# Kernel tuning notes

Hardware: AMD Instinct MI355X
Metric: run time of the kernel (lower is better)

Reference implementation:

```python
import math
import jax, jax.numpy as jnp
import numpy as np

HALF_PI = math.pi / 2
TWOR_SCALE = 1.0 / math.log(2.0)
B, C, L, K = 32, 2, 262144, 4


def setup_inputs() -> dict:
    key = jax.random.key(0)
    ks = jax.random.split(key, 6)
    return {
        "input_signal": jax.random.normal(ks[0], (B, C, L), jnp.float32),
        "twoR": jax.random.normal(ks[1], (B, K), jnp.float32),
        "G": jax.random.normal(ks[2], (B, K), jnp.float32),
        "c_hp": jax.random.normal(ks[3], (B, K), jnp.float32),
        "c_bp": jax.random.normal(ks[4], (B, K), jnp.float32),
        "c_lp": jax.random.normal(ks[5], (B, K), jnp.float32),
    }


def get_biquad_coefficients(twoR, G, c_hp, c_bp, c_lp):
    # each arg: (B, K)
    G2 = G * G
    b0 = c_hp + c_bp * G + c_lp * G2
    b1 = -2.0 * c_hp + 2.0 * c_lp * G2
    b2 = c_hp - c_bp * G + c_lp * G2
    a0 = 1.0 + G2 + twoR * G
    a1 = 2.0 * G2 - 2.0
    a2 = 1.0 + G2 - twoR * G
    return jnp.stack([b0, b1, b2], -1), jnp.stack([a0, a1, a2], -1)  # (B,K,3)


def _biquad_cascade(x, Bs, As):
    # x: (B,C,L); Bs, As: (B,1,K,3) -- broadcast over channels.
    # Direct-form II transposed, cascaded in series over K filters.
    Bs = Bs / As[..., :1]
    As = As / As[..., :1]
    b_, c_ = x.shape[0], x.shape[1]
    y = x
    num_filters = Bs.shape[2]
    for k in range(num_filters):
        b0, b1, b2 = Bs[:, :, k, 0], Bs[:, :, k, 1], Bs[:, :, k, 2]  # (B,1)
        a1, a2 = As[:, :, k, 1], As[:, :, k, 2]  # (B,1)

        def step(carry, xt):
            s1, s2 = carry
            yt = b0 * xt + s1              # (B,C)
            s1n = b1 * xt - a1 * yt + s2
            s2n = b2 * xt - a2 * yt
            return (s1n, s2n), yt

        init = (jnp.zeros((b_, c_), y.dtype), jnp.zeros((b_, c_), y.dtype))
        _, yT = jax.lax.scan(step, init, jnp.moveaxis(y, -1, 0))  # (L,B,C)
        y = jnp.moveaxis(yT, 0, -1)
    return y


def reference(input_signal, twoR, G, c_hp, c_bp, c_lp):
    G = jnp.tan(HALF_PI * jax.nn.sigmoid(G))
    twoR = TWOR_SCALE * jax.nn.softplus(twoR) + 0.01
    Bs, As = get_biquad_coefficients(twoR, G, c_hp, c_bp, c_lp)  # (B,K,3)
    Bs, As = Bs[:, None], As[:, None]  # unsqueeze(1): (B,1,K,3)
    return _biquad_cascade(input_signal, Bs, As)
```

## Files before the change

kernel.cpp:

```cpp
#include <hip/hip_runtime.h>
#include <math.h>

#define B_N 32
#define C_N 2
#define L_N 262144
#define K_N 4
#define NSEQ (B_N * C_N)
#define CHUNK 64
#define THREADS 128
#define BLKSAMP (CHUNK * THREADS)
#define NBLK_SEQ (L_N / BLKSAMP)
#define NBLK_TOT (NSEQ * NBLK_SEQ)
#define NLVL 7
#define ROWP (CHUNK + 1)

#define WS_COEF 0
#define WS_PL   (B_N * 20)
#define WS_PBLK (WS_PL + B_N * NLVL * 64)
#define WS_AGG  (WS_PBLK + B_N * 64)

__global__ __launch_bounds__(64) void svf_prep(
    const float* __restrict__ twoR, const float* __restrict__ Graw,
    const float* __restrict__ c_hp, const float* __restrict__ c_bp,
    const float* __restrict__ c_lp, float* __restrict__ ws)
{
    const int b = blockIdx.x;
    const int t = threadIdx.x;
    __shared__ double cf[K_N][5];
    __shared__ double M[8][8];

    if (t < K_N) {
        const int k = t;
        double g  = (double)Graw[b * K_N + k];
        double tr = (double)twoR[b * K_N + k];
        double hp = (double)c_hp[b * K_N + k];
        double bp = (double)c_bp[b * K_N + k];
        double lp = (double)c_lp[b * K_N + k];
        double sg = 1.0 / (1.0 + exp(-g));
        double G  = tan(1.5707963267948966 * sg);
        double R  = log1p(exp(tr)) * 1.4426950408889634 + 0.01;
        double G2 = G * G;
        double b0 = hp + bp * G + lp * G2;
        double b1 = -2.0 * hp + 2.0 * lp * G2;
        double b2 = hp - bp * G + lp * G2;
        double a0 = 1.0 + G2 + R * G;
        double a1 = 2.0 * G2 - 2.0;
        double a2 = 1.0 + G2 - R * G;
        cf[k][0] = b0 / a0; cf[k][1] = b1 / a0; cf[k][2] = b2 / a0;
        cf[k][3] = a1 / a0; cf[k][4] = a2 / a0;
    }
    __syncthreads();

    if (t < 20) ws[WS_COEF + b * 20 + t] = (float)cf[t / 5][t % 5];

    if (t < 8) {
        double s[8];
        #pragma unroll
        for (int i = 0; i < 8; ++i) s[i] = (i == t) ? 1.0 : 0.0;
        double in = 0.0;
        #pragma unroll
        for (int k = 0; k < K_N; ++k) {
            double y   = cf[k][0] * in + s[2 * k];
            double s1n = cf[k][1] * in - cf[k][3] * y + s[2 * k + 1];
            double s2n = cf[k][2] * in - cf[k][4] * y;
            s[2 * k] = s1n; s[2 * k + 1] = s2n; in = y;
        }
        #pragma unroll
        for (int i = 0; i < 8; ++i) M[i][t] = s[i];
    }
    __syncthreads();

    const int i = t >> 3, j = t & 7;
    for (int p = 1; p <= 13; ++p) {
        double acc = 0.0;
        #pragma unroll
        for (int k = 0; k < 8; ++k) acc += M[i][k] * M[k][j];
        __syncthreads();
        M[i][j] = acc;
        __syncthreads();
        if (p >= 6 && p <= 12) ws[WS_PL + (b * NLVL + (p - 6)) * 64 + t] = (float)acc;
        if (p == 13)           ws[WS_PBLK + b * 64 + t] = (float)acc;
    }
}

__device__ __forceinline__ float cascade_step(const float cf[20], float s[8], float in)
{
    #pragma unroll
    for (int k = 0; k < K_N; ++k) {
        float y  = fmaf(cf[k * 5 + 0], in, s[2 * k]);
        float t1 = fmaf(cf[k * 5 + 1], in, s[2 * k + 1]);
        float n1 = fmaf(-cf[k * 5 + 3], y, t1);
        float n2 = fmaf(-cf[k * 5 + 4], y, cf[k * 5 + 2] * in);
        s[2 * k] = n1; s[2 * k + 1] = n2;
        in = y;
    }
    return in;
}

__device__ __forceinline__ void load_tile(const float* __restrict__ xg,
                                          float* __restrict__ xt, int tid)
{
    #pragma unroll
    for (int k = 0; k < BLKSAMP / 4 / THREADS; ++k) {
        const int g0 = (tid + k * THREADS) * 4;
        float4 v = ((const float4*)xg)[tid + k * THREADS];
        const int a = (g0 >> 6) * ROWP + (g0 & 63);
        xt[a] = v.x; xt[a + 1] = v.y; xt[a + 2] = v.z; xt[a + 3] = v.w;
    }
}

__global__ __launch_bounds__(THREADS) void svf_pass1(
    const float* __restrict__ x, const float* __restrict__ ws,
    float* __restrict__ out)
{
    const int seq = blockIdx.x >> 5;
    const int blk = blockIdx.x & (NBLK_SEQ - 1);
    const int tid = threadIdx.x;
    const int b   = seq >> 1;

    __shared__ float xt[THREADS * ROWP];
    __shared__ float Pm[NLVL][64];
    __shared__ float tb[THREADS][9];

    for (int q = tid; q < NLVL * 64; q += THREADS)
        Pm[q >> 6][q & 63] = ws[WS_PL + b * NLVL * 64 + q];

    float cf[20];
    #pragma unroll
    for (int q = 0; q < 20; ++q) cf[q] = ws[WS_COEF + b * 20 + q];

    const size_t base = (size_t)seq * L_N + (size_t)blk * BLKSAMP;
    load_tile(x + base, xt, tid);
    __syncthreads();

    float t[8] = {0, 0, 0, 0, 0, 0, 0, 0};
    const float* xr = &xt[tid * ROWP];
    #pragma unroll 4
    for (int j = 0; j < CHUNK; ++j) (void)cascade_step(cf, t, xr[j]);

    for (int l = 0; l < NLVL; ++l) {
        const int d = 1 << l;
        #pragma unroll
        for (int q = 0; q < 8; ++q) tb[tid][q] = t[q];
        __syncthreads();
        float prev[8];
        const bool have = (tid >= d);
        if (have) {
            #pragma unroll
            for (int q = 0; q < 8; ++q) prev[q] = tb[tid - d][q];
        }
        __syncthreads();
        if (have) {
            #pragma unroll
            for (int r = 0; r < 8; ++r) {
                float acc = t[r];
                #pragma unroll
                for (int c = 0; c < 8; ++c)
                    acc = fmaf(Pm[l][r * 8 + c], prev[c], acc);
                t[r] = acc;
            }
        }
    }

    float e[8] = {0, 0, 0, 0, 0, 0, 0, 0};
    if (tid > 0) {
        #pragma unroll
        for (int q = 0; q < 8; ++q) e[q] = tb[tid - 1][q];
    }
    float4* eo = (float4*)(out + base);
    eo[2 * tid]     = make_float4(e[0], e[1], e[2], e[3]);
    eo[2 * tid + 1] = make_float4(e[4], e[5], e[6], e[7]);

    if (tid == THREADS - 1) {
        float* agg = (float*)ws + WS_AGG + (size_t)blockIdx.x * 8;
        #pragma unroll
        for (int q = 0; q < 8; ++q) agg[q] = t[q];
    }
}

__global__ __launch_bounds__(64) void svf_scanb(float* __restrict__ ws)
{
    const int seq = threadIdx.x;
    const int b   = seq >> 1;
    float P[64];
    #pragma unroll
    for (int q = 0; q < 64; ++q) P[q] = ws[WS_PBLK + b * 64 + q];

    float* agg = ws + WS_AGG + (size_t)seq * NBLK_SEQ * 8;

    float t[8] = {0, 0, 0, 0, 0, 0, 0, 0};
    for (int j = 0; j < NBLK_SEQ; ++j) {
        float f[8];
        #pragma unroll
        for (int q = 0; q < 8; ++q) f[q] = agg[j * 8 + q];
        #pragma unroll
        for (int q = 0; q < 8; ++q) agg[j * 8 + q] = t[q];
        float nt[8];
        #pragma unroll
        for (int r = 0; r < 8; ++r) {
            float acc = f[r];
            #pragma unroll
            for (int c = 0; c < 8; ++c) acc = fmaf(P[r * 8 + c], t[c], acc);
            nt[r] = acc;
        }
        #pragma unroll
        for (int q = 0; q < 8; ++q) t[q] = nt[q];
    }
}

__global__ __launch_bounds__(THREADS) void svf_pass2(
    const float* __restrict__ x, const float* __restrict__ ws,
    float* __restrict__ out)
{
    const int seq = blockIdx.x >> 5;
    const int blk = blockIdx.x & (NBLK_SEQ - 1);
    const int tid = threadIdx.x;
    const int b   = seq >> 1;

    __shared__ float xt[THREADS * ROWP];
    __shared__ float Pm[NLVL][64];

    for (int q = tid; q < NLVL * 64; q += THREADS)
        Pm[q >> 6][q & 63] = ws[WS_PL + b * NLVL * 64 + q];

    float cf[20];
    #pragma unroll
    for (int q = 0; q < 20; ++q) cf[q] = ws[WS_COEF + b * 20 + q];

    const size_t base = (size_t)seq * L_N + (size_t)blk * BLKSAMP;

    const float4* eo = (const float4*)(out + base);
    float4 e0 = eo[2 * tid], e1 = eo[2 * tid + 1];

    const float* sbp = ws + WS_AGG + (size_t)blockIdx.x * 8;
    float v[8];
    #pragma unroll
    for (int q = 0; q < 8; ++q) v[q] = sbp[q];

    load_tile(x + base, xt, tid);

    __syncthreads();
    #pragma unroll
    for (int l = 0; l < NLVL; ++l) {
        if ((tid >> l) & 1) {
            float nv[8];
            #pragma unroll
            for (int r = 0; r < 8; ++r) {
                float acc = 0.0f;
                #pragma unroll
                for (int c = 0; c < 8; ++c)
                    acc = fmaf(Pm[l][r * 8 + c], v[c], acc);
                nv[r] = acc;
            }
            #pragma unroll
            for (int q = 0; q < 8; ++q) v[q] = nv[q];
        }
    }

    float s[8] = {e0.x + v[0], e0.y + v[1], e0.z + v[2], e0.w + v[3],
                  e1.x + v[4], e1.y + v[5], e1.z + v[6], e1.w + v[7]};

    float* xr = &xt[tid * ROWP];
    #pragma unroll 4
    for (int j = 0; j < CHUNK; ++j) xr[j] = cascade_step(cf, s, xr[j]);
    __syncthreads();

    #pragma unroll
    for (int k = 0; k < BLKSAMP / 4 / THREADS; ++k) {
        const int g0 = (tid + k * THREADS) * 4;
        const int a = (g0 >> 6) * ROWP + (g0 & 63);
        ((float4*)(out + base))[tid + k * THREADS] =
            make_float4(xt[a], xt[a + 1], xt[a + 2], xt[a + 3]);
    }
}

extern "C" void kernel_launch(void* const* d_in, const int* in_sizes, int n_in,
                              void* d_out, int out_size, void* d_ws, size_t ws_size,
                              hipStream_t stream)
{
    (void)in_sizes; (void)n_in; (void)out_size; (void)ws_size;
    const float* x    = (const float*)d_in[0];
    const float* twoR = (const float*)d_in[1];
    const float* G    = (const float*)d_in[2];
    const float* chp  = (const float*)d_in[3];
    const float* cbp  = (const float*)d_in[4];
    const float* clp  = (const float*)d_in[5];
    float* out = (float*)d_out;
    float* ws  = (float*)d_ws;

    svf_prep <<<B_N, 64, 0, stream>>>(twoR, G, chp, cbp, clp, ws);
    svf_pass1<<<NBLK_TOT, THREADS, 0, stream>>>(x, ws, out);
    svf_scanb<<<1, 64, 0, stream>>>(ws);
    svf_pass2<<<NBLK_TOT, THREADS, 0, stream>>>(x, ws, out);
}
```

Baseline: 172.6 us.

## Halve chunk length, double threads, stage tiles through small per-wave shared window

Changes the per-thread chunk from 64 to 32 samples and the block size from 128 to 256 threads, adding one more scan level and its precomputed transition matrix. Shared-memory use shrinks by staging the input and output tile one wave at a time through a small padded window into register arrays. Register-resident chunks and full unrolling remove the large LDS tile to raise occupancy and shorten the serial recurrence per thread. The cost is more synchronisation rounds, a deeper block scan, and higher register pressure from the 32-element arrays.

```diff
diff --git a/kernel.cpp b/kernel.cpp
--- a/kernel.cpp
+++ b/kernel.cpp
@@ -6,13 +6,13 @@
 #define L_N 262144
 #define K_N 4
 #define NSEQ (B_N * C_N)
-#define CHUNK 64
-#define THREADS 128
+#define CHUNK 32
+#define THREADS 256
 #define BLKSAMP (CHUNK * THREADS)
 #define NBLK_SEQ (L_N / BLKSAMP)
 #define NBLK_TOT (NSEQ * NBLK_SEQ)
-#define NLVL 7
-#define ROWP (CHUNK + 1)
+#define NLVL 8
+#define ROWW 33
 
 #define WS_COEF 0
 #define WS_PL   (B_N * 20)
@@ -78,7 +78,7 @@
         __syncthreads();
         M[i][j] = acc;
         __syncthreads();
-        if (p >= 6 && p <= 12) ws[WS_PL + (b * NLVL + (p - 6)) * 64 + t] = (float)acc;
+        if (p >= 5 && p <= 12) ws[WS_PL + (b * NLVL + (p - 5)) * 64 + t] = (float)acc;
         if (p == 13)           ws[WS_PBLK + b * 64 + t] = (float)acc;
     }
 }
@@ -97,15 +97,29 @@
     return in;
 }
 
-__device__ __forceinline__ void load_tile(const float* __restrict__ xg,
-                                          float* __restrict__ xt, int tid)
-{
-    #pragma unroll
-    for (int k = 0; k < BLKSAMP / 4 / THREADS; ++k) {
-        const int g0 = (tid + k * THREADS) * 4;
-        float4 v = ((const float4*)xg)[tid + k * THREADS];
-        const int a = (g0 >> 6) * ROWP + (g0 & 63);
-        xt[a] = v.x; xt[a + 1] = v.y; xt[a + 2] = v.z; xt[a + 3] = v.w;
+__device__ __forceinline__ void stage_load(const float4* __restrict__ xg4,
+                                           float* __restrict__ win,
+                                           float* __restrict__ xr, int tid)
+{
+    float4 v4[8];
+    #pragma unroll
+    for (int j = 0; j < 8; ++j) v4[j] = xg4[tid + j * THREADS];
+    const int myw = tid >> 6, lane = tid & 63;
+    #pragma unroll
+    for (int r = 0; r < 4; ++r) {
+        #pragma unroll
+        for (int h = 0; h < 2; ++h) {
+            const int fw = tid + h * THREADS;
+            const int a  = (fw >> 3) * ROWW + (fw & 7) * 4;
+            float4 v = v4[2 * r + h];
+            win[a] = v.x; win[a + 1] = v.y; win[a + 2] = v.z; win[a + 3] = v.w;
+        }
+        __syncthreads();
+        if (myw == r) {
+            #pragma unroll
+            for (int j = 0; j < CHUNK; ++j) xr[j] = win[lane * ROWW + j];
+        }
+        __syncthreads();
     }
 }
 
@@ -118,36 +132,34 @@
     const int tid = threadIdx.x;
     const int b   = seq >> 1;
 
-    __shared__ float xt[THREADS * ROWP];
-    __shared__ float Pm[NLVL][64];
-    __shared__ float tb[THREADS][9];
+    __shared__ float smem[THREADS * 9];
+    __shared__ float Pm[NLVL * 64];
 
     for (int q = tid; q < NLVL * 64; q += THREADS)
-        Pm[q >> 6][q & 63] = ws[WS_PL + b * NLVL * 64 + q];
+        Pm[q] = ws[WS_PL + b * NLVL * 64 + q];
 
     float cf[20];
     #pragma unroll
     for (int q = 0; q < 20; ++q) cf[q] = ws[WS_COEF + b * 20 + q];
 
     const size_t base = (size_t)seq * L_N + (size_t)blk * BLKSAMP;
-    load_tile(x + base, xt, tid);
-    __syncthreads();
+    float xr[CHUNK];
+    stage_load((const float4*)(x + base), smem, xr, tid);
 
     float t[8] = {0, 0, 0, 0, 0, 0, 0, 0};
-    const float* xr = &xt[tid * ROWP];
-    #pragma unroll 4
+    #pragma unroll
     for (int j = 0; j < CHUNK; ++j) (void)cascade_step(cf, t, xr[j]);
 
     for (int l = 0; l < NLVL; ++l) {
         const int d = 1 << l;
         #pragma unroll
-        for (int q = 0; q < 8; ++q) tb[tid][q] = t[q];
+        for (int q = 0; q < 8; ++q) smem[tid * 9 + q] = t[q];
         __syncthreads();
         float prev[8];
         const bool have = (tid >= d);
         if (have) {
             #pragma unroll
-            for (int q = 0; q < 8; ++q) prev[q] = tb[tid - d][q];
+            for (int q = 0; q < 8; ++q) prev[q] = smem[(tid - d) * 9 + q];
         }
         __syncthreads();
         if (have) {
@@ -156,16 +168,19 @@
                 float acc = t[r];
                 #pragma unroll
                 for (int c = 0; c < 8; ++c)
-                    acc = fmaf(Pm[l][r * 8 + c], prev[c], acc);
+                    acc = fmaf(Pm[l * 64 + r * 8 + c], prev[c], acc);
                 t[r] = acc;
             }
         }
     }
+    #pragma unroll
+    for (int q = 0; q < 8; ++q) smem[tid * 9 + q] = t[q];
+    __syncthreads();
 
     float e[8] = {0, 0, 0, 0, 0, 0, 0, 0};
     if (tid > 0) {
         #pragma unroll
-        for (int q = 0; q < 8; ++q) e[q] = tb[tid - 1][q];
+        for (int q = 0; q < 8; ++q) e[q] = smem[(tid - 1) * 9 + q];
     }
     float4* eo = (float4*)(out + base);
     eo[2 * tid]     = make_float4(e[0], e[1], e[2], e[3]);
@@ -217,15 +232,8 @@
     const int tid = threadIdx.x;
     const int b   = seq >> 1;
 
-    __shared__ float xt[THREADS * ROWP];
-    __shared__ float Pm[NLVL][64];
-
-    for (int q = tid; q < NLVL * 64; q += THREADS)
-        Pm[q >> 6][q & 63] = ws[WS_PL + b * NLVL * 64 + q];
-
-    float cf[20];
-    #pragma unroll
-    for (int q = 0; q < 20; ++q) cf[q] = ws[WS_COEF + b * 20 + q];
+    __shared__ float smem[THREADS * 9];
+    __shared__ float Pm[NLVL * 64];
 
     const size_t base = (size_t)seq * L_N + (size_t)blk * BLKSAMP;
 
@@ -237,9 +245,16 @@
     #pragma unroll
     for (int q = 0; q < 8; ++q) v[q] = sbp[q];
 
-    load_tile(x + base, xt, tid);
-
-    __syncthreads();
+    for (int q = tid; q < NLVL * 64; q += THREADS)
+        Pm[q] = ws[WS_PL + b * NLVL * 64 + q];
+
+    float cf[20];
+    #pragma unroll
+    for (int q = 0; q < 20; ++q) cf[q] = ws[WS_COEF + b * 20 + q];
+
+    float xr[CHUNK];
+    stage_load((const float4*)(x + base), smem, xr, tid);
+
     #pragma unroll
     for (int l = 0; l < NLVL; ++l) {
         if ((tid >> l) & 1) {
@@ -249,7 +264,7 @@
                 float acc = 0.0f;
                 #pragma unroll
                 for (int c = 0; c < 8; ++c)
-                    acc = fmaf(Pm[l][r * 8 + c], v[c], acc);
+                    acc = fmaf(Pm[l * 64 + r * 8 + c], v[c], acc);
                 nv[r] = acc;
             }
             #pragma unroll
@@ -260,17 +275,25 @@
     float s[8] = {e0.x + v[0], e0.y + v[1], e0.z + v[2], e0.w + v[3],
                   e1.x + v[4], e1.y + v[5], e1.z + v[6], e1.w + v[7]};
 
-    float* xr = &xt[tid * ROWP];
-    #pragma unroll 4
+    #pragma unroll
     for (int j = 0; j < CHUNK; ++j) xr[j] = cascade_step(cf, s, xr[j]);
-    __syncthreads();
-
-    #pragma unroll
-    for (int k = 0; k < BLKSAMP / 4 / THREADS; ++k) {
-        const int g0 = (tid + k * THREADS) * 4;
-        const int a = (g0 >> 6) * ROWP + (g0 & 63);
-        ((float4*)(out + base))[tid + k * THREADS] =
-            make_float4(xt[a], xt[a + 1], xt[a + 2], xt[a + 3]);
+
+    const int myw = tid >> 6, lane = tid & 63;
+    float4* og4 = (float4*)(out + base);
+    for (int r = 0; r < 4; ++r) {
+        if (myw == r) {
+            #pragma unroll
+            for (int j = 0; j < CHUNK; ++j) smem[lane * ROWW + j] = xr[j];
+        }
+        __syncthreads();
+        #pragma unroll
+        for (int h = 0; h < 2; ++h) {
+            const int fw = tid + h * THREADS;
+            const int a  = (fw >> 3) * ROWW + (fw & 7) * 4;
+            og4[r * 512 + fw] =
+                make_float4(smem[a], smem[a + 1], smem[a + 2], smem[a + 3]);
+        }
+        __syncthreads();
     }
 }
 
```

After: 163.9 us. 5.1% less time.
